# Kernel optimization log

Hardware: AMD Instinct MI355X
Metric: run time of the kernel (lower is better)

The kernel has to match this reference:

```python
import jax, jax.numpy as jnp
import numpy as np

B, I, D = 8192, 1000, 1000   # batch of candidates, rated items, item feature dim
E, ATT, D1, D2 = 64, 16, 64, 32  # embed size, attention hidden, MLP dense1/dense2


def setup_inputs() -> dict:
    key = jax.random.key(0)
    ks = jax.random.split(key, 16)
    init = lambda k, shape, fan_in: (jax.random.normal(k, shape, jnp.float32) / np.sqrt(fan_in))
    return {
        "candidate_items": jax.random.normal(ks[0], (B, D), jnp.float32),
        "rated_items": jax.random.normal(ks[1], (I, D), jnp.float32),
        "user_matrix": jax.random.uniform(ks[2], (B, I), jnp.float32),
        # item_embeddings: Linear(D, E)
        "We": init(ks[3], (E, D), D), "be": jnp.zeros((E,), jnp.float32),
        # AttentionNet: Linear(2E, ATT) -> ReLU -> Linear(ATT, 1)
        "Wa1": init(ks[4], (ATT, 2 * E), 2 * E), "ba1": jnp.zeros((ATT,), jnp.float32),
        "Wa2": init(ks[5], (1, ATT), ATT), "ba2": jnp.zeros((1,), jnp.float32),
        # MLP: Linear(2E, D1) -> ReLU -> Linear(D1, D2) -> ReLU -> Linear(D2, 1)
        "Wm1": init(ks[6], (D1, 2 * E), 2 * E), "bm1": jnp.zeros((D1,), jnp.float32),
        "Wm2": init(ks[7], (D2, D1), D1), "bm2": jnp.zeros((D2,), jnp.float32),
        "Wm3": init(ks[8], (1, D2), D2), "bm3": jnp.zeros((1,), jnp.float32),
    }


def reference(candidate_items, rated_items, user_matrix,
              We, be, Wa1, ba1, Wa2, ba2, Wm1, bm1, Wm2, bm2, Wm3, bm3):
    # item embeddings
    e_c = candidate_items @ We.T + be                    # [B, E]
    # rated embeddings are .detach()'d in the original
    e_r = jax.lax.stop_gradient(rated_items @ We.T + be) # [I, E]
    e_c_sg = jax.lax.stop_gradient(e_c)                  # detached for attention

    # Additive attention over concat([cand, rated]): split Wa1 into cand/rated halves
    # so the per-i loop becomes one broadcasted op producing [B, I, ATT].
    W1c, W1r = Wa1[:, :E], Wa1[:, E:]
    h = jax.nn.relu(e_c_sg @ W1c.T[:, None, :].reshape(1, 1, -1).reshape(E, ATT)[None][0] if False else
                    (e_c_sg @ W1c.T)[:, None, :] + (e_r @ W1r.T)[None, :, :] + ba1)  # [B, I, ATT]
    scores = jnp.einsum('bia,a->bi', h, Wa2[0]) + ba2[0]  # [B, I]
    att = jax.nn.softmax(scores, axis=1)                  # [B, I]

    # attention-weighted user profile -> user embedding
    user_emb = (att * user_matrix) @ e_r                  # [B, E]

    # MLP head (dropout inactive: eval mode)
    x = jnp.concatenate([e_c, user_emb], axis=1)          # [B, 2E]
    x = jax.nn.relu(x @ Wm1.T + bm1)
    x = jax.nn.relu(x @ Wm2.T + bm2)
    return x @ Wm3.T + bm3                                # [B, 1]
```

## Files before the change

kernel.cpp:

```cpp
#include <hip/hip_runtime.h>

typedef unsigned short u16;
typedef unsigned int   u32;
typedef float f32x4  __attribute__((ext_vector_type(4)));
typedef short bf16x8 __attribute__((ext_vector_type(8)));
typedef short s16x4  __attribute__((ext_vector_type(4)));

__device__ __forceinline__ u16 f2b_rne(float x) {
    u32 u = __float_as_uint(x);
    return (u16)((u + 0x7fffu + ((u >> 16) & 1u)) >> 16);
}
__device__ __forceinline__ float b2f(u16 u) { return __uint_as_float((u32)u << 16); }
__device__ __forceinline__ void split1(float x, u16& h, u16& l) {
    h = f2b_rne(x);
    l = f2b_rne(x - b2f(h));
}
__device__ __forceinline__ void mk_frag(f32x4 a, f32x4 b, bf16x8& hi, bf16x8& lo) {
#pragma unroll
    for (int j = 0; j < 4; ++j) { u16 h, l; split1(a[j], h, l); hi[j] = (short)h; lo[j] = (short)l; }
#pragma unroll
    for (int j = 0; j < 4; ++j) { u16 h, l; split1(b[j], h, l); hi[4+j] = (short)h; lo[4+j] = (short)l; }
}

__device__ __forceinline__ void stage16(
    const float* __restrict__ X, int i0, int Mrows,
    u16* XH, u16* XL, int wv, int lane)
{
    const int arow = min(i0 + wv, Mrows - 1);
    const float* xr = X + (size_t)arow * 1000;
#pragma unroll
    for (int j = 0; j < 4; ++j) {
        const int k4 = lane + j * 64;
        if (k4 < 250) {
            f32x4 v = *(const f32x4*)(xr + k4 * 4);
            s16x4 h4, l4;
#pragma unroll
            for (int jj = 0; jj < 4; ++jj) {
                u16 hh, ll; split1(v[jj], hh, ll);
                h4[jj] = (short)hh; l4[jj] = (short)ll;
            }
            *(s16x4*)(XH + wv * 1008 + k4 * 4) = h4;
            *(s16x4*)(XL + wv * 1008 + k4 * 4) = l4;
        }
    }
}

__device__ __forceinline__ f32x4 gemm_tile_f32(
    const float* __restrict__ X, int i0, int Mrows,
    const float* __restrict__ We,
    u16* XH, u16* XL, int wv, int lane, int l15, int q)
{
    stage16(X, i0, Mrows, XH, XL, wv, lane);
    __syncthreads();

    const int ct = wv & 3, h = wv >> 2;
    f32x4 acc = {0.f, 0.f, 0.f, 0.f};
    const u16* ahp = XH + l15 * 1008;
    const u16* alp = XL + l15 * 1008;
    const float* wr = We + (size_t)(ct * 16 + l15) * 1000;

    const int kc0 = h * 256;
    const int kc1 = (h == 3) ? 992 : kc0 + 256;
    for (int kc = kc0; kc < kc1; kc += 32) {
        bf16x8 ah = *(const bf16x8*)(ahp + kc + q * 8);
        bf16x8 al = *(const bf16x8*)(alp + kc + q * 8);
        bf16x8 bh, bl;
        mk_frag(*(const f32x4*)(wr + kc + q * 8), *(const f32x4*)(wr + kc + q * 8 + 4), bh, bl);
        acc = __builtin_amdgcn_mfma_f32_16x16x32_bf16(ah, bh, acc, 0, 0, 0);
        acc = __builtin_amdgcn_mfma_f32_16x16x32_bf16(ah, bl, acc, 0, 0, 0);
        acc = __builtin_amdgcn_mfma_f32_16x16x32_bf16(al, bh, acc, 0, 0, 0);
    }
    if (h == 3) {
        bf16x8 ah = {0,0,0,0,0,0,0,0}, al = {0,0,0,0,0,0,0,0};
        bf16x8 bh = {0,0,0,0,0,0,0,0}, bl = {0,0,0,0,0,0,0,0};
        if (q == 0) {
            ah = *(const bf16x8*)(ahp + 992);
            al = *(const bf16x8*)(alp + 992);
            mk_frag(*(const f32x4*)(wr + 992), *(const f32x4*)(wr + 996), bh, bl);
        }
        acc = __builtin_amdgcn_mfma_f32_16x16x32_bf16(ah, bh, acc, 0, 0, 0);
        acc = __builtin_amdgcn_mfma_f32_16x16x32_bf16(ah, bl, acc, 0, 0, 0);
        acc = __builtin_amdgcn_mfma_f32_16x16x32_bf16(al, bh, acc, 0, 0, 0);
    }
    __syncthreads();
    return acc;
}

__global__ __launch_bounds__(1024, 8) void kprep(
    const float* __restrict__ rated, const float* __restrict__ We,
    const float* __restrict__ be, const float* __restrict__ Wa1,
    const float* __restrict__ Wm1,
    u16* __restrict__ er_th, float* __restrict__ ar, u16* __restrict__ Wm1b,
    u16* __restrict__ Weh, u16* __restrict__ Wel)
{
    const int blk = blockIdx.x;
    if (blk == 63) {
        for (int idx = threadIdx.x; idx < 8192; idx += 1024)
            Wm1b[idx] = f2b_rne(Wm1[idx]);
        return;
    }
    if (blk >= 64) {
        const int g = (blk - 64) * 1024 + threadIdx.x;
        const int e0 = g * 16;
        if (e0 < 64000) {
#pragma unroll
            for (int j = 0; j < 4; ++j) {
                f32x4 v = *(const f32x4*)(We + e0 + j * 4);
                s16x4 h4, l4;
#pragma unroll
                for (int jj = 0; jj < 4; ++jj) {
                    u16 hh, ll; split1(v[jj], hh, ll);
                    h4[jj] = (short)hh; l4[jj] = (short)ll;
                }
                *(s16x4*)(Weh + e0 + j * 4) = h4;
                *(s16x4*)(Wel + e0 + j * 4) = l4;
            }
        }
        return;
    }

    __shared__ __attribute__((aligned(16))) u16 PL[2 * 16 * 1008];
    float* Sf = (float*)PL;
    u16* XH = PL;
    u16* XL = PL + 16 * 1008;

    const int t    = threadIdx.x;
    const int wv   = t >> 6;
    const int lane = t & 63;
    const int l15  = lane & 15;
    const int q    = lane >> 4;
    const int i0r  = blk * 16;

    f32x4 a2 = gemm_tile_f32(rated, i0r, 1000, We, XH, XL, wv, lane, l15, q);
    const int ct = wv & 3, h = wv >> 2;
#pragma unroll
    for (int r = 0; r < 4; ++r)
        Sf[h * 1024 + (q * 4 + r) * 64 + ct * 16 + l15] = a2[r];
    __syncthreads();
    {
        const int b = t >> 6, e = t & 63;
        float v = be[e] + Sf[b * 64 + e] + Sf[1024 + b * 64 + e]
                        + Sf[2048 + b * 64 + e] + Sf[3072 + b * 64 + e];
        if (i0r + b < 1000) er_th[(size_t)e * 1000 + (i0r + b)] = f2b_rne(v);
        Sf[4096 + b * 68 + e] = v;
    }
    __syncthreads();
    if (wv == 0) {
        f32x4 a3 = {0.f, 0.f, 0.f, 0.f};
#pragma unroll
        for (int kc = 0; kc < 64; kc += 32) {
            const float* ap = Sf + 4096 + l15 * 68 + kc + q * 8;
            const float* bp = Wa1 + l15 * 128 + 64 + kc + q * 8;
            bf16x8 ah, al, bh, bl;
            mk_frag(*(const f32x4*)ap, *(const f32x4*)(ap + 4), ah, al);
            mk_frag(*(const f32x4*)bp, *(const f32x4*)(bp + 4), bh, bl);
            a3 = __builtin_amdgcn_mfma_f32_16x16x32_bf16(ah, bh, a3, 0, 0, 0);
            a3 = __builtin_amdgcn_mfma_f32_16x16x32_bf16(ah, bl, a3, 0, 0, 0);
            a3 = __builtin_amdgcn_mfma_f32_16x16x32_bf16(al, bh, a3, 0, 0, 0);
        }
#pragma unroll
        for (int r = 0; r < 4; ++r) {
            int i = i0r + q * 4 + r;
            if (i < 1000) ar[(size_t)i * 16 + l15] = a3[r];
        }
    }
}

__global__ __launch_bounds__(1024, 8) void kmain(
    const float* __restrict__ cand,
    const u16* __restrict__ Weh, const u16* __restrict__ Wel,
    const float* __restrict__ be,
    const float* __restrict__ Wa1, const float* __restrict__ ba1,
    const float* __restrict__ Wa2, const float* __restrict__ um,
    const float* __restrict__ bm1,
    const float* __restrict__ Wm2, const float* __restrict__ bm2,
    const float* __restrict__ Wm3, const float* __restrict__ bm3,
    const u16* __restrict__ er_th, const float* __restrict__ ar,
    const u16* __restrict__ Wm1b, float* __restrict__ out)
{
    __shared__ __attribute__((aligned(16))) u16 PL[2 * 16 * 1008];
    __shared__ float ECT[16 * 64];
    __shared__ float ACL[256];
    __shared__ float SUMS[16];
    __shared__ __attribute__((aligned(16))) u16 XB16[16 * 136];
    float* Sf = (float*)PL;
    u16*  XH  = PL;
    u16*  XL  = PL + 16 * 1008;
    u16*  S16 = PL;

    const int t    = threadIdx.x;
    const int wv   = t >> 6;
    const int lane = t & 63;
    const int l15  = lane & 15;
    const int q    = lane >> 4;
    const int b0   = blockIdx.x * 16;

    {
        stage16(cand, b0, 8192, XH, XL, wv, lane);
        __syncthreads();

        const int ct = wv & 3, h = wv >> 2;
        f32x4 acc = {0.f, 0.f, 0.f, 0.f};
        const u16* ahp = XH + l15 * 1008;
        const u16* alp = XL + l15 * 1008;
        const u16* whp = Weh + (size_t)(ct * 16 + l15) * 1000;
        const u16* wlp = Wel + (size_t)(ct * 16 + l15) * 1000;

        const int kc0 = h * 256;
        const int kc1 = (h == 3) ? 992 : kc0 + 256;
#pragma unroll 2
        for (int kc = kc0; kc < kc1; kc += 32) {
            bf16x8 ah = *(const bf16x8*)(ahp + kc + q * 8);
            bf16x8 al = *(const bf16x8*)(alp + kc + q * 8);
            bf16x8 bh = *(const bf16x8*)(whp + kc + q * 8);
            bf16x8 bl = *(const bf16x8*)(wlp + kc + q * 8);
            acc = __builtin_amdgcn_mfma_f32_16x16x32_bf16(ah, bh, acc, 0, 0, 0);
            acc = __builtin_amdgcn_mfma_f32_16x16x32_bf16(ah, bl, acc, 0, 0, 0);
            acc = __builtin_amdgcn_mfma_f32_16x16x32_bf16(al, bh, acc, 0, 0, 0);
        }
        if (h == 3) {
            bf16x8 ah = {0,0,0,0,0,0,0,0}, al = {0,0,0,0,0,0,0,0};
            bf16x8 bh = {0,0,0,0,0,0,0,0}, bl = {0,0,0,0,0,0,0,0};
            if (q == 0) {
                ah = *(const bf16x8*)(ahp + 992);
                al = *(const bf16x8*)(alp + 992);
                bh = *(const bf16x8*)(whp + 992);
                bl = *(const bf16x8*)(wlp + 992);
            }
            acc = __builtin_amdgcn_mfma_f32_16x16x32_bf16(ah, bh, acc, 0, 0, 0);
            acc = __builtin_amdgcn_mfma_f32_16x16x32_bf16(ah, bl, acc, 0, 0, 0);
            acc = __builtin_amdgcn_mfma_f32_16x16x32_bf16(al, bh, acc, 0, 0, 0);
        }
        __syncthreads();
#pragma unroll
        for (int r = 0; r < 4; ++r)
            Sf[h * 1024 + (q * 4 + r) * 64 + ct * 16 + l15] = acc[r];
        __syncthreads();
        const int b = t >> 6, e = t & 63;
        ECT[b * 64 + e] = be[e] + Sf[b * 64 + e] + Sf[1024 + b * 64 + e]
                                + Sf[2048 + b * 64 + e] + Sf[3072 + b * 64 + e];
        __syncthreads();
    }


    if (t < 256) {
        const int a = t & 15, b = t >> 4;
        float acc = ba1[a];
        const float* w = Wa1 + a * 128;
#pragma unroll 8
        for (int e = 0; e < 64; ++e) acc += ECT[b * 64 + e] * w[e];
        ACL[b * 16 + a] = acc;
    }
    __syncthreads();

    {
        const int i = t;
        if (i < 1000) {
            const f32x4* a4 = (const f32x4*)(ar + (size_t)i * 16);
            f32x4 r0 = a4[0], r1 = a4[1], r2 = a4[2], r3 = a4[3];
            float w2[16];
#pragma unroll
            for (int a = 0; a < 16; ++a) w2[a] = Wa2[a];
#pragma unroll 4
            for (int b = 0; b < 16; ++b) {
                const f32x4* ac4 = (const f32x4*)(ACL + b * 16);
                f32x4 c0 = ac4[0], c1 = ac4[1], c2 = ac4[2], c3 = ac4[3];
                float s0 = 0.f, s1 = 0.f;
                s0 += fmaxf(c0[0] + r0[0], 0.f) * w2[0];
                s1 += fmaxf(c0[1] + r0[1], 0.f) * w2[1];
                s0 += fmaxf(c0[2] + r0[2], 0.f) * w2[2];
                s1 += fmaxf(c0[3] + r0[3], 0.f) * w2[3];
                s0 += fmaxf(c1[0] + r1[0], 0.f) * w2[4];
                s1 += fmaxf(c1[1] + r1[1], 0.f) * w2[5];
                s0 += fmaxf(c1[2] + r1[2], 0.f) * w2[6];
                s1 += fmaxf(c1[3] + r1[3], 0.f) * w2[7];
                s0 += fmaxf(c2[0] + r2[0], 0.f) * w2[8];
                s1 += fmaxf(c2[1] + r2[1], 0.f) * w2[9];
                s0 += fmaxf(c2[2] + r2[2], 0.f) * w2[10];
                s1 += fmaxf(c2[3] + r2[3], 0.f) * w2[11];
                s0 += fmaxf(c3[0] + r3[0], 0.f) * w2[12];
                s1 += fmaxf(c3[1] + r3[1], 0.f) * w2[13];
                s0 += fmaxf(c3[2] + r3[2], 0.f) * w2[14];
                s1 += fmaxf(c3[3] + r3[3], 0.f) * w2[15];
                S16[b * 1032 + i] = f2b_rne(s0 + s1);
            }
        }
    }
    __syncthreads();

    {
        const int b = t >> 6, g = t & 63;
        float sv[16], uv[16];
        const float* umr = um + (size_t)(b0 + b) * 1000;
#pragma unroll
        for (int k = 0; k < 16; ++k) {
            int i = g + 64 * k;
            uv[k] = (i < 1000) ? umr[i] : 0.f;
        }
#pragma unroll
        for (int k = 0; k < 16; ++k) {
            int i = g + 64 * k;
            sv[k] = (i < 1000) ? b2f(S16[b * 1032 + i]) : -1e30f;
        }
        float m = -1e30f;
#pragma unroll
        for (int k = 0; k < 16; ++k) m = fmaxf(m, sv[k]);
#pragma unroll
        for (int k = 1; k < 64; k <<= 1) m = fmaxf(m, __shfl_xor(m, k));
        float sum = 0.f;
#pragma unroll
        for (int k = 0; k < 16; ++k) {
            int i = g + 64 * k;
            if (i < 1000) {
                float w = __expf(sv[k] - m);
                sum += w;
                S16[b * 1032 + i] = f2b_rne(w * uv[k]);
            }
        }
#pragma unroll
        for (int k = 1; k < 64; k <<= 1) sum += __shfl_xor(sum, k);
        if (g == 0) SUMS[b] = 1.0f / sum;
    }
    __syncthreads();

    {
        const int et = wv & 3, h = wv >> 2;
        const u16* php = S16 + l15 * 1032;
        const u16* bhp = er_th + (size_t)(et * 16 + l15) * 1000;
        f32x4 acc = {0.f, 0.f, 0.f, 0.f};

        const int kc0 = h * 256;
        const int kc1 = (h == 3) ? 992 : kc0 + 256;
        for (int kc = kc0; kc < kc1; kc += 32) {
            bf16x8 ah = *(const bf16x8*)(php + kc + q * 8);
            bf16x8 bh = *(const bf16x8*)(bhp + kc + q * 8);
            acc = __builtin_amdgcn_mfma_f32_16x16x32_bf16(ah, bh, acc, 0, 0, 0);
        }
        if (h == 3) {
            bf16x8 ah = {0,0,0,0,0,0,0,0}, bh = {0,0,0,0,0,0,0,0};
            if (q == 0) {
                ah = *(const bf16x8*)(php + 992);
                bh = *(const bf16x8*)(bhp + 992);
            }
            acc = __builtin_amdgcn_mfma_f32_16x16x32_bf16(ah, bh, acc, 0, 0, 0);
        }
        __syncthreads();
#pragma unroll
        for (int r = 0; r < 4; ++r)
            Sf[h * 1024 + (q * 4 + r) * 64 + et * 16 + l15] = acc[r];
    }
    __syncthreads();

    {
        const int b = t >> 6, e = t & 63;
        float v = (Sf[b * 64 + e] + Sf[1024 + b * 64 + e]
                 + Sf[2048 + b * 64 + e] + Sf[3072 + b * 64 + e]) * SUMS[b];
        XB16[b * 136 + 64 + e] = f2b_rne(v);
        XB16[b * 136 + e] = f2b_rne(ECT[b * 64 + e]);
    }
    __syncthreads();

    {
        const int nt = wv & 3, kh = wv >> 2;
        bf16x8 ah = *(const bf16x8*)(XB16 + l15 * 136 + kh * 32 + q * 8);
        bf16x8 bh = *(const bf16x8*)(Wm1b + (size_t)(nt * 16 + l15) * 128 + kh * 32 + q * 8);
        f32x4 acc = {0.f, 0.f, 0.f, 0.f};
        acc = __builtin_amdgcn_mfma_f32_16x16x32_bf16(ah, bh, acc, 0, 0, 0);
#pragma unroll
        for (int r = 0; r < 4; ++r)
            Sf[kh * 1024 + (q * 4 + r) * 64 + nt * 16 + l15] = acc[r];
    }
    __syncthreads();

    {
        const int b = t >> 6, o = t & 63;
        float a = bm1[o] + Sf[b * 64 + o] + Sf[1024 + b * 64 + o]
                + Sf[2048 + b * 64 + o] + Sf[3072 + b * 64 + o];
        Sf[4096 + b * 64 + o] = fmaxf(a, 0.f);
    }
    __syncthreads();

    {
        const int b = t >> 6, j = t & 63;
        if (j < 32) {
            float a = bm2[j];
            const float* wr = Wm2 + j * 64;
            const float* x = Sf + 4096 + b * 64;
#pragma unroll 8
            for (int k = 0; k < 64; ++k) a += x[k] * wr[k];
            Sf[5120 + b * 32 + j] = fmaxf(a, 0.f);
        }
    }
    __syncthreads();

    {
        const int b = t >> 6, j = t & 63;
        float p = (j < 32) ? Sf[5120 + b * 32 + j] * Wm3[j] : 0.f;
#pragma unroll
        for (int kk = 1; kk < 64; kk <<= 1) p += __shfl_xor(p, kk);
        if (j == 0) out[b0 + b] = p + bm3[0];
    }
}

extern "C" void kernel_launch(void* const* d_in, const int* in_sizes, int n_in,
                              void* d_out, int out_size, void* d_ws, size_t ws_size,
                              hipStream_t stream) {
    const float* cand  = (const float*)d_in[0];
    const float* rated = (const float*)d_in[1];
    const float* um    = (const float*)d_in[2];
    const float* We    = (const float*)d_in[3];
    const float* be    = (const float*)d_in[4];
    const float* Wa1   = (const float*)d_in[5];
    const float* ba1   = (const float*)d_in[6];
    const float* Wa2   = (const float*)d_in[7];
    const float* Wm1   = (const float*)d_in[9];
    const float* bm1   = (const float*)d_in[10];
    const float* Wm2   = (const float*)d_in[11];
    const float* bm2   = (const float*)d_in[12];
    const float* Wm3   = (const float*)d_in[13];
    const float* bm3   = (const float*)d_in[14];

    char* w = (char*)d_ws;
    float* arw   = (float*)(w);
    u16*   er_th = (u16*)(w + 64000);
    u16*   wm1b  = (u16*)(w + 192000);
    u16*   weh   = (u16*)(w + 208384);
    u16*   wel   = (u16*)(w + 336384);
    float* out   = (float*)d_out;

    kprep<<<dim3(68),  dim3(1024), 0, stream>>>(rated, We, be, Wa1, Wm1,
                                                er_th, arw, wm1b, weh, wel);
    kmain<<<dim3(512), dim3(1024), 0, stream>>>(cand, weh, wel, be, Wa1, ba1,
                                                Wa2, um, bm1, Wm2, bm2, Wm3,
                                                bm3, er_th, arw, wm1b, out);
}
```

Baseline: 158.1 us.

## Rewrite ReLU-dot via abs identity, split MFMA accumulators, prefetch user row

```diff
diff --git a/kernel.cpp b/kernel.cpp
--- a/kernel.cpp
+++ b/kernel.cpp
@@ -54,7 +54,7 @@
     __syncthreads();
 
     const int ct = wv & 3, h = wv >> 2;
-    f32x4 acc = {0.f, 0.f, 0.f, 0.f};
+    f32x4 a0 = {0.f,0.f,0.f,0.f}, a1 = a0, a2 = a0;
     const u16* ahp = XH + l15 * 1008;
     const u16* alp = XL + l15 * 1008;
     const float* wr = We + (size_t)(ct * 16 + l15) * 1000;
@@ -66,9 +66,9 @@
         bf16x8 al = *(const bf16x8*)(alp + kc + q * 8);
         bf16x8 bh, bl;
         mk_frag(*(const f32x4*)(wr + kc + q * 8), *(const f32x4*)(wr + kc + q * 8 + 4), bh, bl);
-        acc = __builtin_amdgcn_mfma_f32_16x16x32_bf16(ah, bh, acc, 0, 0, 0);
-        acc = __builtin_amdgcn_mfma_f32_16x16x32_bf16(ah, bl, acc, 0, 0, 0);
-        acc = __builtin_amdgcn_mfma_f32_16x16x32_bf16(al, bh, acc, 0, 0, 0);
+        a0 = __builtin_amdgcn_mfma_f32_16x16x32_bf16(ah, bh, a0, 0, 0, 0);
+        a1 = __builtin_amdgcn_mfma_f32_16x16x32_bf16(ah, bl, a1, 0, 0, 0);
+        a2 = __builtin_amdgcn_mfma_f32_16x16x32_bf16(al, bh, a2, 0, 0, 0);
     }
     if (h == 3) {
         bf16x8 ah = {0,0,0,0,0,0,0,0}, al = {0,0,0,0,0,0,0,0};
@@ -78,11 +78,14 @@
             al = *(const bf16x8*)(alp + 992);
             mk_frag(*(const f32x4*)(wr + 992), *(const f32x4*)(wr + 996), bh, bl);
         }
-        acc = __builtin_amdgcn_mfma_f32_16x16x32_bf16(ah, bh, acc, 0, 0, 0);
-        acc = __builtin_amdgcn_mfma_f32_16x16x32_bf16(ah, bl, acc, 0, 0, 0);
-        acc = __builtin_amdgcn_mfma_f32_16x16x32_bf16(al, bh, acc, 0, 0, 0);
-    }
-    __syncthreads();
+        a0 = __builtin_amdgcn_mfma_f32_16x16x32_bf16(ah, bh, a0, 0, 0, 0);
+        a1 = __builtin_amdgcn_mfma_f32_16x16x32_bf16(ah, bl, a1, 0, 0, 0);
+        a2 = __builtin_amdgcn_mfma_f32_16x16x32_bf16(al, bh, a2, 0, 0, 0);
+    }
+    __syncthreads();
+    f32x4 acc;
+#pragma unroll
+    for (int r = 0; r < 4; ++r) acc[r] = a0[r] + a1[r] + a2[r];
     return acc;
 }
 
@@ -181,6 +184,7 @@
     __shared__ __attribute__((aligned(16))) u16 PL[2 * 16 * 1008];
     __shared__ float ECT[16 * 64];
     __shared__ float ACL[256];
+    __shared__ float BB[16];
     __shared__ float SUMS[16];
     __shared__ __attribute__((aligned(16))) u16 XB16[16 * 136];
     float* Sf = (float*)PL;
@@ -200,7 +204,7 @@
         __syncthreads();
 
         const int ct = wv & 3, h = wv >> 2;
-        f32x4 acc = {0.f, 0.f, 0.f, 0.f};
+        f32x4 a0 = {0.f,0.f,0.f,0.f}, a1 = a0, a2 = a0;
         const u16* ahp = XH + l15 * 1008;
         const u16* alp = XL + l15 * 1008;
         const u16* whp = Weh + (size_t)(ct * 16 + l15) * 1000;
@@ -214,9 +218,9 @@
             bf16x8 al = *(const bf16x8*)(alp + kc + q * 8);
             bf16x8 bh = *(const bf16x8*)(whp + kc + q * 8);
             bf16x8 bl = *(const bf16x8*)(wlp + kc + q * 8);
-            acc = __builtin_amdgcn_mfma_f32_16x16x32_bf16(ah, bh, acc, 0, 0, 0);
-            acc = __builtin_amdgcn_mfma_f32_16x16x32_bf16(ah, bl, acc, 0, 0, 0);
-            acc = __builtin_amdgcn_mfma_f32_16x16x32_bf16(al, bh, acc, 0, 0, 0);
+            a0 = __builtin_amdgcn_mfma_f32_16x16x32_bf16(ah, bh, a0, 0, 0, 0);
+            a1 = __builtin_amdgcn_mfma_f32_16x16x32_bf16(ah, bl, a1, 0, 0, 0);
+            a2 = __builtin_amdgcn_mfma_f32_16x16x32_bf16(al, bh, a2, 0, 0, 0);
         }
         if (h == 3) {
             bf16x8 ah = {0,0,0,0,0,0,0,0}, al = {0,0,0,0,0,0,0,0};
@@ -227,21 +231,20 @@
                 bh = *(const bf16x8*)(whp + 992);
                 bl = *(const bf16x8*)(wlp + 992);
             }
-            acc = __builtin_amdgcn_mfma_f32_16x16x32_bf16(ah, bh, acc, 0, 0, 0);
-            acc = __builtin_amdgcn_mfma_f32_16x16x32_bf16(ah, bl, acc, 0, 0, 0);
-            acc = __builtin_amdgcn_mfma_f32_16x16x32_bf16(al, bh, acc, 0, 0, 0);
+            a0 = __builtin_amdgcn_mfma_f32_16x16x32_bf16(ah, bh, a0, 0, 0, 0);
+            a1 = __builtin_amdgcn_mfma_f32_16x16x32_bf16(ah, bl, a1, 0, 0, 0);
+            a2 = __builtin_amdgcn_mfma_f32_16x16x32_bf16(al, bh, a2, 0, 0, 0);
         }
         __syncthreads();
 #pragma unroll
         for (int r = 0; r < 4; ++r)
-            Sf[h * 1024 + (q * 4 + r) * 64 + ct * 16 + l15] = acc[r];
+            Sf[h * 1024 + (q * 4 + r) * 64 + ct * 16 + l15] = a0[r] + a1[r] + a2[r];
         __syncthreads();
         const int b = t >> 6, e = t & 63;
         ECT[b * 64 + e] = be[e] + Sf[b * 64 + e] + Sf[1024 + b * 64 + e]
                                 + Sf[2048 + b * 64 + e] + Sf[3072 + b * 64 + e];
         __syncthreads();
     }
-
 
     if (t < 256) {
         const int a = t & 15, b = t >> 4;
@@ -250,38 +253,59 @@
 #pragma unroll 8
         for (int e = 0; e < 64; ++e) acc += ECT[b * 64 + e] * w[e];
         ACL[b * 16 + a] = acc;
-    }
-    __syncthreads();
+        float p = 0.5f * Wa2[a] * acc;
+        p += __shfl_xor(p, 1);
+        p += __shfl_xor(p, 2);
+        p += __shfl_xor(p, 4);
+        p += __shfl_xor(p, 8);
+        if (a == 0) BB[b] = p;
+    }
+    __syncthreads();
+
+    float uv[16];
+    {
+        const int b = t >> 6, g = t & 63;
+        const float* umr = um + (size_t)(b0 + b) * 1000;
+#pragma unroll
+        for (int k = 0; k < 16; ++k) {
+            int ii = g + 64 * k;
+            uv[k] = (ii < 1000) ? umr[ii] : 0.f;
+        }
+    }
 
     {
         const int i = t;
         if (i < 1000) {
             const f32x4* a4 = (const f32x4*)(ar + (size_t)i * 16);
             f32x4 r0 = a4[0], r1 = a4[1], r2 = a4[2], r3 = a4[3];
-            float w2[16];
-#pragma unroll
-            for (int a = 0; a < 16; ++a) w2[a] = Wa2[a];
+            float w2h[16];
+#pragma unroll
+            for (int a = 0; a < 16; ++a) w2h[a] = 0.5f * Wa2[a];
+            float Bi = w2h[0]*r0[0] + w2h[1]*r0[1] + w2h[2]*r0[2] + w2h[3]*r0[3]
+                     + w2h[4]*r1[0] + w2h[5]*r1[1] + w2h[6]*r1[2] + w2h[7]*r1[3]
+                     + w2h[8]*r2[0] + w2h[9]*r2[1] + w2h[10]*r2[2] + w2h[11]*r2[3]
+                     + w2h[12]*r3[0] + w2h[13]*r3[1] + w2h[14]*r3[2] + w2h[15]*r3[3];
 #pragma unroll 4
             for (int b = 0; b < 16; ++b) {
                 const f32x4* ac4 = (const f32x4*)(ACL + b * 16);
                 f32x4 c0 = ac4[0], c1 = ac4[1], c2 = ac4[2], c3 = ac4[3];
-                float s0 = 0.f, s1 = 0.f;
-                s0 += fmaxf(c0[0] + r0[0], 0.f) * w2[0];
-                s1 += fmaxf(c0[1] + r0[1], 0.f) * w2[1];
-                s0 += fmaxf(c0[2] + r0[2], 0.f) * w2[2];
-                s1 += fmaxf(c0[3] + r0[3], 0.f) * w2[3];
-                s0 += fmaxf(c1[0] + r1[0], 0.f) * w2[4];
-                s1 += fmaxf(c1[1] + r1[1], 0.f) * w2[5];
-                s0 += fmaxf(c1[2] + r1[2], 0.f) * w2[6];
-                s1 += fmaxf(c1[3] + r1[3], 0.f) * w2[7];
-                s0 += fmaxf(c2[0] + r2[0], 0.f) * w2[8];
-                s1 += fmaxf(c2[1] + r2[1], 0.f) * w2[9];
-                s0 += fmaxf(c2[2] + r2[2], 0.f) * w2[10];
-                s1 += fmaxf(c2[3] + r2[3], 0.f) * w2[11];
-                s0 += fmaxf(c3[0] + r3[0], 0.f) * w2[12];
-                s1 += fmaxf(c3[1] + r3[1], 0.f) * w2[13];
-                s0 += fmaxf(c3[2] + r3[2], 0.f) * w2[14];
-                s1 += fmaxf(c3[3] + r3[3], 0.f) * w2[15];
+                float s0 = BB[b] + Bi, s1 = 0.f;
+                s0 += w2h[0]  * fabsf(c0[0] + r0[0]);
+                s1 += w2h[1]  * fabsf(c0[1] + r0[1]);
+                s0 += w2h[2]  * fabsf(c0[2] + r0[2]);
+                s1 += w2h[3]  * fabsf(c0[3] + r0[3]);
+                s0 += w2h[4]  * fabsf(c1[0] + r1[0]);
+                s1 += w2h[5]  * fabsf(c1[1] + r1[1]);
+                s0 += w2h[6]  * fabsf(c1[2] + r1[2]);
+                s1 += w2h[7]  * fabsf(c1[3] + r1[3]);
+                s0 += w2h[8]  * fabsf(c2[0] + r2[0]);
+                s1 += w2h[9]  * fabsf(c2[1] + r2[1]);
+                s0 += w2h[10] * fabsf(c2[2] + r2[2]);
+                s1 += w2h[11] * fabsf(c2[3] + r2[3]);
+                s0 += w2h[12] * fabsf(c3[0] + r3[0]);
+                s1 += w2h[13] * fabsf(c3[1] + r3[1]);
+                s0 += w2h[14] * fabsf(c3[2] + r3[2]);
+                s1 += w2h[15] * fabsf(c3[3] + r3[3]);
                 S16[b * 1032 + i] = f2b_rne(s0 + s1);
             }
         }
@@ -290,13 +314,7 @@
 
     {
         const int b = t >> 6, g = t & 63;
-        float sv[16], uv[16];
-        const float* umr = um + (size_t)(b0 + b) * 1000;
-#pragma unroll
-        for (int k = 0; k < 16; ++k) {
-            int i = g + 64 * k;
-            uv[k] = (i < 1000) ? umr[i] : 0.f;
-        }
+        float sv[16];
 #pragma unroll
         for (int k = 0; k < 16; ++k) {
             int i = g + 64 * k;
@@ -327,14 +345,21 @@
         const int et = wv & 3, h = wv >> 2;
         const u16* php = S16 + l15 * 1032;
         const u16* bhp = er_th + (size_t)(et * 16 + l15) * 1000;
-        f32x4 acc = {0.f, 0.f, 0.f, 0.f};
+        f32x4 aA = {0.f,0.f,0.f,0.f}, aB = aA;
 
         const int kc0 = h * 256;
         const int kc1 = (h == 3) ? 992 : kc0 + 256;
-        for (int kc = kc0; kc < kc1; kc += 32) {
-            bf16x8 ah = *(const bf16x8*)(php + kc + q * 8);
-            bf16x8 bh = *(const bf16x8*)(bhp + kc + q * 8);
-            acc = __builtin_amdgcn_mfma_f32_16x16x32_bf16(ah, bh, acc, 0, 0, 0);
+        for (int kc = kc0; kc < kc1; kc += 64) {
+            {
+                bf16x8 ah = *(const bf16x8*)(php + kc + q * 8);
+                bf16x8 bh = *(const bf16x8*)(bhp + kc + q * 8);
+                aA = __builtin_amdgcn_mfma_f32_16x16x32_bf16(ah, bh, aA, 0, 0, 0);
+            }
+            if (kc + 32 < kc1) {
+                bf16x8 ah = *(const bf16x8*)(php + kc + 32 + q * 8);
+                bf16x8 bh = *(const bf16x8*)(bhp + kc + 32 + q * 8);
+                aB = __builtin_amdgcn_mfma_f32_16x16x32_bf16(ah, bh, aB, 0, 0, 0);
+            }
         }
         if (h == 3) {
             bf16x8 ah = {0,0,0,0,0,0,0,0}, bh = {0,0,0,0,0,0,0,0};
@@ -342,12 +367,12 @@
                 ah = *(const bf16x8*)(php + 992);
                 bh = *(const bf16x8*)(bhp + 992);
             }
-            acc = __builtin_amdgcn_mfma_f32_16x16x32_bf16(ah, bh, acc, 0, 0, 0);
+            aB = __builtin_amdgcn_mfma_f32_16x16x32_bf16(ah, bh, aB, 0, 0, 0);
         }
         __syncthreads();
 #pragma unroll
         for (int r = 0; r < 4; ++r)
-            Sf[h * 1024 + (q * 4 + r) * 64 + et * 16 + l15] = acc[r];
+            Sf[h * 1024 + (q * 4 + r) * 64 + et * 16 + l15] = aA[r] + aB[r];
     }
     __syncthreads();
 
```

After: 189.0 us. 19.5% more time.
